# Kernel optimization log

Hardware: AMD Instinct MI355X
Metric: run time of the kernel (lower is better)

The kernel has to match this reference:

```python
import jax, jax.numpy as jnp
import numpy as np

SEQ, BATCH, IN, RES = 1024, 64, 512, 2048

def setup_inputs() -> dict:
    key = jax.random.key(0)
    k1, k2, k3, k4 = jax.random.split(key, 4)
    x = jax.random.normal(k1, (SEQ, BATCH, IN), dtype=jnp.float32)
    # ESN reservoir weights: untrained random matrices (spectral-radius style scaling)
    W_in = jax.random.normal(k2, (RES, IN), dtype=jnp.float32) * 0.1
    W_hh = jax.random.normal(k3, (RES, RES), dtype=jnp.float32) * (0.9 / jnp.sqrt(RES))
    b = jax.random.normal(k4, (RES,), dtype=jnp.float32) * 0.1
    return {"x": x, "W_in": W_in, "W_hh": W_hh, "b": b}

def reference(x, W_in, W_hh, b):
    # ESNBase.forward -> _forward_type_2 with num_layers=1, unidirectional.
    # h_t = tanh(x_t @ W_in^T + h_{t-1} @ W_hh^T + b)
    batch = x.shape[1]
    h0 = jnp.zeros((batch, W_hh.shape[0]), dtype=x.dtype)
    # Precompute input projection for all steps (parallel GEMM), scan the recurrence.
    xin = jnp.einsum('sbi,ri->sbr', x, W_in) + b  # (seq, batch, res)
    def step(h, u):
        h_new = jnp.tanh(u + h @ W_hh.T)
        return h_new, h_new
    h_n, states = jax.lax.scan(step, h0, xin)
    # output: (seq, batch, num_directions*hidden); h_n: (num_layers*num_directions, batch, hidden)
    return states, h_n[None, :, :]
```

## Files before the change

### kernel.cpp

```cpp
#include <hip/hip_runtime.h>
#include <hip/hip_bf16.h>


#define SEQ  1024
#define NB   64
#define INF  512
#define RES  2048
#define RING 16

typedef float    f32x4 __attribute__((ext_vector_type(4)));
typedef _Float16 f16x8 __attribute__((ext_vector_type(8)));

__device__ __forceinline__ float fast_tanh(float x) {
  const float e = __expf(2.0f * x);
  return 1.0f - 2.0f * __builtin_amdgcn_rcpf(1.0f + e);
}

__global__ __launch_bounds__(256) void xin_gemm(
    const float* __restrict__ X, const float* __restrict__ Win,
    const float* __restrict__ bias, float* __restrict__ U)
{
  __shared__ _Float16 lA[2][128][40];
  __shared__ _Float16 lB[2][128][40];

  const int tid  = threadIdx.x;
  const int lane = tid & 63;
  const int wv   = tid >> 6;
  const int wr   = wv >> 1;
  const int wc   = wv & 1;
  const int m0   = (blockIdx.x >> 4) * 128;
  const int n0   = (blockIdx.x & 15) * 128;

  const int srow = tid >> 1;
  const int sk   = (tid & 1) * 16;

  const int fr = lane & 15;
  const int fk = (lane >> 4) * 8;

  f32x4 acc[4][4] = {};
  float ra[16], rb[16];

  const float* xa_base = X   + (size_t)(m0 + srow) * INF + sk;
  const float* xb_base = Win + (size_t)(n0 + srow) * INF + sk;

#define LOADK(kt) do {                                                     \
    const float* pa = xa_base + (kt) * 32;                                 \
    const float* pb = xb_base + (kt) * 32;                                 \
    *(f32x4*)&ra[0]  = *(const f32x4*)(pa + 0);                            \
    *(f32x4*)&ra[4]  = *(const f32x4*)(pa + 4);                            \
    *(f32x4*)&ra[8]  = *(const f32x4*)(pa + 8);                            \
    *(f32x4*)&ra[12] = *(const f32x4*)(pa + 12);                           \
    *(f32x4*)&rb[0]  = *(const f32x4*)(pb + 0);                            \
    *(f32x4*)&rb[4]  = *(const f32x4*)(pb + 4);                            \
    *(f32x4*)&rb[8]  = *(const f32x4*)(pb + 8);                            \
    *(f32x4*)&rb[12] = *(const f32x4*)(pb + 12);                           \
  } while (0)

#define STOREK(buf) do {                                                   \
    f16x8 h0, h1;                                                          \
    _Pragma("unroll") for (int j = 0; j < 8; ++j) h0[j] = (_Float16)ra[j]; \
    _Pragma("unroll") for (int j = 0; j < 8; ++j) h1[j] = (_Float16)ra[8+j];\
    *(f16x8*)&lA[buf][srow][sk]     = h0;                                  \
    *(f16x8*)&lA[buf][srow][sk + 8] = h1;                                  \
    _Pragma("unroll") for (int j = 0; j < 8; ++j) h0[j] = (_Float16)rb[j]; \
    _Pragma("unroll") for (int j = 0; j < 8; ++j) h1[j] = (_Float16)rb[8+j];\
    *(f16x8*)&lB[buf][srow][sk]     = h0;                                  \
    *(f16x8*)&lB[buf][srow][sk + 8] = h1;                                  \
  } while (0)

#define COMPUTE(buf) do {                                                  \
    f16x8 af[4], bf[4];                                                    \
    _Pragma("unroll") for (int mt = 0; mt < 4; ++mt)                       \
      af[mt] = *(const f16x8*)&lA[buf][wr*64 + mt*16 + fr][fk];            \
    _Pragma("unroll") for (int nt = 0; nt < 4; ++nt)                       \
      bf[nt] = *(const f16x8*)&lB[buf][wc*64 + nt*16 + fr][fk];            \
    _Pragma("unroll") for (int mt = 0; mt < 4; ++mt)                       \
      _Pragma("unroll") for (int nt = 0; nt < 4; ++nt)                     \
        acc[mt][nt] = __builtin_amdgcn_mfma_f32_16x16x32_f16(              \
            af[mt], bf[nt], acc[mt][nt], 0, 0, 0);                         \
  } while (0)

  LOADK(0);
  STOREK(0);
  __syncthreads();

#pragma unroll 1
  for (int kt = 0; kt < 16; ++kt) {
    const int buf = kt & 1;
    if (kt < 15) LOADK(kt + 1);
    COMPUTE(buf);
    if (kt < 15) STOREK(buf ^ 1);
    __syncthreads();
  }

#pragma unroll
  for (int mt = 0; mt < 4; ++mt) {
    const int row = m0 + wr*64 + mt*16 + (lane >> 4) * 4;
#pragma unroll
    for (int nt = 0; nt < 4; ++nt) {
      const int col = n0 + wc*64 + nt*16 + fr;
      const float bv = bias[col];
#pragma unroll
      for (int i = 0; i < 4; ++i)
        U[(size_t)(row + i) * RES + col] = acc[mt][nt][i] + bv;
    }
  }
#undef LOADK
#undef STOREK
#undef COMPUTE
}

__global__ __launch_bounds__(512, 1) void esn_recur(
    const float* __restrict__ Whh, float* __restrict__ states,
    float* __restrict__ hn, _Float16* __restrict__ ring,
    unsigned* __restrict__ flags)
{
  __shared__ f32x4 red0[8][64];
  __shared__ f32x4 red1[8][64];

  const int tid  = threadIdx.x;
  const int lane = tid & 63;
  const int wv   = tid >> 6;
  const int q    = wv;

  const int bid = blockIdx.x;
  const int xg  = bid & 7;
  const int bg  = xg >> 1;
  const int cg  = ((xg & 1) << 5) | (bid >> 3);
  const int b0  = bg * 16;
  const int c0  = cg * 32;

  const int fr = lane & 15;
  const int fk = (lane >> 4) * 8;

  f16x8 wf[2][8];
#pragma unroll
  for (int ct = 0; ct < 2; ++ct) {
#pragma unroll
    for (int ks = 0; ks < 8; ++ks) {
      const float* wsrc = Whh + (size_t)(c0 + ct*16 + fr) * RES
                        + q*256 + ks*32 + fk;
      const f32x4 w0 = *(const f32x4*)(wsrc);
      const f32x4 w1 = *(const f32x4*)(wsrc + 4);
      f16x8 f;
#pragma unroll
      for (int j = 0; j < 4; ++j) { f[j] = (_Float16)w0[j]; f[4+j] = (_Float16)w1[j]; }
      wf[ct][ks] = f;
    }
  }

  unsigned* const fb = flags + bg * (128 * 32);

  for (int s = 0; s < SEQ; ++s) {
    f32x4 a0 = {0.f, 0.f, 0.f, 0.f}, a1 = {0.f, 0.f, 0.f, 0.f};

    float u[4];
    if (wv < 2) {
      const float* up = states + (size_t)s * NB * RES;
      const int col = c0 + wv * 16 + fr;
#pragma unroll
      for (int i = 0; i < 4; ++i)
        u[i] = up[(size_t)(b0 + (lane >> 4) * 4 + i) * RES + col];
    }

    if (s > 0) {
      const _Float16* hp = ring + (size_t)((s - 1) & (RING - 1)) * NB * RES
                         + (size_t)(b0 + fr) * RES + q * 256 + fk;
      f16x8 hv[8];
      for (;;) {
#pragma unroll
        for (int ks = 0; ks < 8; ++ks) {
          union { unsigned long long w[2]; f16x8 v; } au;
          au.w[0] = __hip_atomic_load((const unsigned long long*)(hp + ks*32),
                                      __ATOMIC_RELAXED, __HIP_MEMORY_SCOPE_AGENT);
          au.w[1] = __hip_atomic_load((const unsigned long long*)(hp + ks*32 + 4),
                                      __ATOMIC_RELAXED, __HIP_MEMORY_SCOPE_AGENT);
          hv[ks] = au.v;
        }
        f16x8 t0 = hv[0] + hv[1], t1 = hv[2] + hv[3];
        f16x8 t2 = hv[4] + hv[5], t3 = hv[6] + hv[7];
        f16x8 ss = (t0 + t1) + (t2 + t3);
        union { f16x8 v; unsigned w[4]; } su; su.v = ss;
        unsigned bad = 0;
#pragma unroll
        for (int j = 0; j < 4; ++j) {
          bad |= ((su.w[j] & 0x7C00u) == 0x7C00u);
          bad |= (((su.w[j] >> 16) & 0x7C00u) == 0x7C00u);
        }
        if (!__any(bad)) break;
      }
#pragma unroll
      for (int ks = 0; ks < 8; ++ks) {
        a0 = __builtin_amdgcn_mfma_f32_16x16x32_f16(hv[ks], wf[0][ks], a0, 0, 0, 0);
        a1 = __builtin_amdgcn_mfma_f32_16x16x32_f16(hv[ks], wf[1][ks], a1, 0, 0, 0);
      }
    }

    red0[q][lane] = a0;
    red1[q][lane] = a1;
    __syncthreads();

    const bool barrier_step = ((s & 7) == 7) && (s != SEQ - 1);

    if (wv < 2) {
      const f32x4 (* __restrict__ rp)[64] = wv ? red1 : red0;
      f32x4 acc = rp[0][lane];
#pragma unroll
      for (int j = 1; j < 8; ++j) acc += rp[j][lane];

      float* up = states + (size_t)s * NB * RES;
      unsigned short* hc16 = (unsigned short*)(ring
                           + (size_t)(s & (RING - 1)) * NB * RES);
      const int col = c0 + wv * 16 + fr;
#pragma unroll
      for (int i = 0; i < 4; ++i) {
        const int b = b0 + (lane >> 4) * 4 + i;
        const size_t off = (size_t)b * RES + col;
        const float v = fast_tanh(u[i] + acc[i]);
        up[off] = v;
        const _Float16 vh = (_Float16)v;
        __hip_atomic_store(&hc16[off], __builtin_bit_cast(unsigned short, vh),
                           __ATOMIC_RELAXED, __HIP_MEMORY_SCOPE_AGENT);
        if (s == SEQ - 1) hn[off] = v;
      }
      asm volatile("s_waitcnt vmcnt(0)" ::: "memory");

      if (barrier_step) {
#pragma unroll
        for (int d = 1; d <= 8; ++d) {
          unsigned short* pz = (unsigned short*)(ring
                             + (size_t)((s + d) & (RING - 1)) * NB * RES);
#pragma unroll
          for (int i = 0; i < 4; ++i) {
            const size_t off = (size_t)(b0 + (lane >> 4) * 4 + i) * RES + col;
            __hip_atomic_store(&pz[off], (unsigned short)0x7F7Fu,
                               __ATOMIC_RELAXED, __HIP_MEMORY_SCOPE_AGENT);
          }
        }
        asm volatile("s_waitcnt vmcnt(0)" ::: "memory");
        if (lane == 0)
          __hip_atomic_store(fb + (wv * 64 + cg) * 32, (unsigned)((s >> 3) + 1),
                             __ATOMIC_RELAXED, __HIP_MEMORY_SCOPE_AGENT);
      }
    } else if (wv == 2 && barrier_step) {
      const unsigned tgt = (unsigned)((s >> 3) + 1);
      for (;;) {
        const unsigned va = __hip_atomic_load(fb + lane * 32,
                              __ATOMIC_RELAXED, __HIP_MEMORY_SCOPE_AGENT);
        const unsigned vb = __hip_atomic_load(fb + (64 + lane) * 32,
                              __ATOMIC_RELAXED, __HIP_MEMORY_SCOPE_AGENT);
        if (__all((va >= tgt) & (vb >= tgt))) break;
      }
    }
    __syncthreads();
  }
}

extern "C" void kernel_launch(void* const* d_in, const int* in_sizes, int n_in,
                              void* d_out, int out_size, void* d_ws, size_t ws_size,
                              hipStream_t stream) {
  const float* x    = (const float*)d_in[0];
  const float* W_in = (const float*)d_in[1];
  const float* W_hh = (const float*)d_in[2];
  const float* bias = (const float*)d_in[3];

  float* states = (float*)d_out;
  float* hn     = states + (size_t)SEQ * NB * RES;

  _Float16* ring  = (_Float16*)d_ws;
  unsigned* flags = (unsigned*)((char*)d_ws
                  + (size_t)RING * NB * RES * sizeof(_Float16));

  hipMemsetAsync(ring, 0x7F, (size_t)RING * NB * RES * sizeof(_Float16), stream);
  hipMemsetAsync(flags, 0, (size_t)4 * 128 * 32 * sizeof(unsigned), stream);

  xin_gemm<<<dim3(512 * 16), dim3(256), 0, stream>>>(x, W_in, bias, states);
  esn_recur<<<dim3(256), dim3(512), 0, stream>>>(W_hh, states, hn, ring, flags);
}
```

Baseline: 6.679 ms.

## Replace flag barriers with ring-slot poisoning and LDS-staged hidden state

Reworks the persistent recurrence kernel's partition. Each block now owns 8 batch rows and 64 columns. Waves cooperatively load the previous hidden state into LDS and then feed MFMA from LDS, split into four K-quarters with a cross-wave reduction. The periodic global flag barrier is removed. Instead, spare waves re-poison the ring slot four steps ahead every step, and the ring shrinks to 8 slots. This cuts global polling and the 8-step group sync, but it relies on the 4-step lead being enough to avoid races. It also wastes half the MFMA rows, since only 8 of the 16 rows are valid.

```diff
diff --git a/kernel.cpp b/kernel.cpp
--- a/kernel.cpp
+++ b/kernel.cpp
@@ -6,7 +6,7 @@
 #define NB   64
 #define INF  512
 #define RES  2048
-#define RING 16
+#define RING 8
 
 typedef float    f32x4 __attribute__((ext_vector_type(4)));
 typedef _Float16 f16x8 __attribute__((ext_vector_type(8)));
@@ -110,76 +110,70 @@
 #undef COMPUTE
 }
 
-__global__ __launch_bounds__(512, 1) void esn_recur(
+__global__ __launch_bounds__(512, 2) void esn_recur(
     const float* __restrict__ Whh, float* __restrict__ states,
-    float* __restrict__ hn, _Float16* __restrict__ ring,
-    unsigned* __restrict__ flags)
+    float* __restrict__ hn, _Float16* __restrict__ ring)
 {
-  __shared__ f32x4 red0[8][64];
-  __shared__ f32x4 red1[8][64];
+  __shared__ _Float16 hl[8 * 2056];
+  __shared__ f32x4    red[2][3][2][2][64];
 
   const int tid  = threadIdx.x;
   const int lane = tid & 63;
   const int wv   = tid >> 6;
-  const int q    = wv;
+  const int kQ   = wv >> 1;
+  const int ctH  = wv & 1;
 
   const int bid = blockIdx.x;
-  const int xg  = bid & 7;
-  const int bg  = xg >> 1;
-  const int cg  = ((xg & 1) << 5) | (bid >> 3);
-  const int b0  = bg * 16;
-  const int c0  = cg * 32;
+  const int g   = bid & 7;
+  const int b0  = g * 8;
+  const int c0  = (bid >> 3) * 64;
 
   const int fr = lane & 15;
   const int fk = (lane >> 4) * 8;
 
-  f16x8 wf[2][8];
-#pragma unroll
-  for (int ct = 0; ct < 2; ++ct) {
-#pragma unroll
-    for (int ks = 0; ks < 8; ++ks) {
-      const float* wsrc = Whh + (size_t)(c0 + ct*16 + fr) * RES
-                        + q*256 + ks*32 + fk;
-      const f32x4 w0 = *(const f32x4*)(wsrc);
-      const f32x4 w1 = *(const f32x4*)(wsrc + 4);
+  f16x8 wf[2][16];
+#pragma unroll 1
+  for (int ct2 = 0; ct2 < 2; ++ct2)
+#pragma unroll
+    for (int ks = 0; ks < 16; ++ks) {
+      const float* src = Whh + (size_t)(c0 + (ctH*2 + ct2)*16 + fr) * RES
+                       + kQ*512 + ks*32 + fk;
+      const f32x4 w0 = *(const f32x4*)src;
+      const f32x4 w1 = *(const f32x4*)(src + 4);
       f16x8 f;
 #pragma unroll
       for (int j = 0; j < 4; ++j) { f[j] = (_Float16)w0[j]; f[4+j] = (_Float16)w1[j]; }
-      wf[ct][ks] = f;
-    }
-  }
-
-  unsigned* const fb = flags + bg * (128 * 32);
+      wf[ct2][ks] = f;
+    }
+
+  const bool epi = (kQ == 0) && ((lane >> 4) < 2);
 
   for (int s = 0; s < SEQ; ++s) {
-    f32x4 a0 = {0.f, 0.f, 0.f, 0.f}, a1 = {0.f, 0.f, 0.f, 0.f};
-
-    float u[4];
-    if (wv < 2) {
+    float u[2][4];
+    if (epi) {
       const float* up = states + (size_t)s * NB * RES;
-      const int col = c0 + wv * 16 + fr;
-#pragma unroll
-      for (int i = 0; i < 4; ++i)
-        u[i] = up[(size_t)(b0 + (lane >> 4) * 4 + i) * RES + col];
-    }
-
+#pragma unroll
+      for (int ct2 = 0; ct2 < 2; ++ct2) {
+        const int col = c0 + (ctH*2 + ct2)*16 + fr;
+#pragma unroll
+        for (int i = 0; i < 4; ++i)
+          u[ct2][i] = up[(size_t)(b0 + (lane >> 4)*4 + i) * RES + col];
+      }
+    }
+
+    unsigned long long d[8];
     if (s > 0) {
-      const _Float16* hp = ring + (size_t)((s - 1) & (RING - 1)) * NB * RES
-                         + (size_t)(b0 + fr) * RES + q * 256 + fk;
-      f16x8 hv[8];
+      const _Float16* hp = ring + (size_t)((s - 1) & (RING - 1)) * (NB * RES)
+                         + (size_t)(b0 + wv) * RES + lane * 32;
       for (;;) {
 #pragma unroll
-        for (int ks = 0; ks < 8; ++ks) {
-          union { unsigned long long w[2]; f16x8 v; } au;
-          au.w[0] = __hip_atomic_load((const unsigned long long*)(hp + ks*32),
-                                      __ATOMIC_RELAXED, __HIP_MEMORY_SCOPE_AGENT);
-          au.w[1] = __hip_atomic_load((const unsigned long long*)(hp + ks*32 + 4),
-                                      __ATOMIC_RELAXED, __HIP_MEMORY_SCOPE_AGENT);
-          hv[ks] = au.v;
-        }
-        f16x8 t0 = hv[0] + hv[1], t1 = hv[2] + hv[3];
-        f16x8 t2 = hv[4] + hv[5], t3 = hv[6] + hv[7];
-        f16x8 ss = (t0 + t1) + (t2 + t3);
+        for (int k = 0; k < 8; ++k)
+          d[k] = __hip_atomic_load((const unsigned long long*)hp + k,
+                                   __ATOMIC_RELAXED, __HIP_MEMORY_SCOPE_AGENT);
+        union { unsigned long long q[2]; f16x8 v; } p0, p1, p2, p3;
+        p0.q[0]=d[0]; p0.q[1]=d[1]; p1.q[0]=d[2]; p1.q[1]=d[3];
+        p2.q[0]=d[4]; p2.q[1]=d[5]; p3.q[0]=d[6]; p3.q[1]=d[7];
+        const f16x8 ss = (p0.v + p1.v) + (p2.v + p3.v);
         union { f16x8 v; unsigned w[4]; } su; su.v = ss;
         unsigned bad = 0;
 #pragma unroll
@@ -189,70 +183,71 @@
         }
         if (!__any(bad)) break;
       }
-#pragma unroll
-      for (int ks = 0; ks < 8; ++ks) {
-        a0 = __builtin_amdgcn_mfma_f32_16x16x32_f16(hv[ks], wf[0][ks], a0, 0, 0, 0);
-        a1 = __builtin_amdgcn_mfma_f32_16x16x32_f16(hv[ks], wf[1][ks], a1, 0, 0, 0);
-      }
-    }
-
-    red0[q][lane] = a0;
-    red1[q][lane] = a1;
+      _Float16* dst = hl + wv * 2056 + lane * 32;
+#pragma unroll
+      for (int k = 0; k < 4; ++k) {
+        union { unsigned long long q[2]; f16x8 v; } p;
+        p.q[0] = d[2*k]; p.q[1] = d[2*k + 1];
+        *(f16x8*)(dst + k * 8) = p.v;
+      }
+    }
     __syncthreads();
 
-    const bool barrier_step = ((s & 7) == 7) && (s != SEQ - 1);
-
-    if (wv < 2) {
-      const f32x4 (* __restrict__ rp)[64] = wv ? red1 : red0;
-      f32x4 acc = rp[0][lane];
-#pragma unroll
-      for (int j = 1; j < 8; ++j) acc += rp[j][lane];
-
-      float* up = states + (size_t)s * NB * RES;
-      unsigned short* hc16 = (unsigned short*)(ring
-                           + (size_t)(s & (RING - 1)) * NB * RES);
-      const int col = c0 + wv * 16 + fr;
-#pragma unroll
-      for (int i = 0; i < 4; ++i) {
-        const int b = b0 + (lane >> 4) * 4 + i;
-        const size_t off = (size_t)b * RES + col;
-        const float v = fast_tanh(u[i] + acc[i]);
-        up[off] = v;
-        const _Float16 vh = (_Float16)v;
-        __hip_atomic_store(&hc16[off], __builtin_bit_cast(unsigned short, vh),
-                           __ATOMIC_RELAXED, __HIP_MEMORY_SCOPE_AGENT);
-        if (s == SEQ - 1) hn[off] = v;
-      }
-      asm volatile("s_waitcnt vmcnt(0)" ::: "memory");
-
-      if (barrier_step) {
-#pragma unroll
-        for (int d = 1; d <= 8; ++d) {
-          unsigned short* pz = (unsigned short*)(ring
-                             + (size_t)((s + d) & (RING - 1)) * NB * RES);
+    f32x4 acc0 = {0.f, 0.f, 0.f, 0.f}, acc1 = {0.f, 0.f, 0.f, 0.f};
+    if (s > 0) {
+      const int  arow = lane & 15;
+      const bool av   = arow < 8;
+      const _Float16* ab = hl + arow * 2056 + kQ * 512 + fk;
+#pragma unroll
+      for (int ks = 0; ks < 16; ++ks) {
+        f16x8 a = {};
+        if (av) a = *(const f16x8*)(ab + ks * 32);
+        acc0 = __builtin_amdgcn_mfma_f32_16x16x32_f16(a, wf[0][ks], acc0, 0, 0, 0);
+        acc1 = __builtin_amdgcn_mfma_f32_16x16x32_f16(a, wf[1][ks], acc1, 0, 0, 0);
+      }
+    }
+
+    if (kQ > 0) {
+      red[s & 1][kQ - 1][ctH][0][lane] = acc0;
+      red[s & 1][kQ - 1][ctH][1][lane] = acc1;
+    }
+    __syncthreads();
+
+    if (kQ == 0) {
+#pragma unroll
+      for (int j = 0; j < 3; ++j) {
+        acc0 += red[s & 1][j][ctH][0][lane];
+        acc1 += red[s & 1][j][ctH][1][lane];
+      }
+      if (epi) {
+        float* up = states + (size_t)s * NB * RES;
+        unsigned short* hc = (unsigned short*)(ring
+                           + (size_t)(s & (RING - 1)) * (NB * RES));
+#pragma unroll
+        for (int ct2 = 0; ct2 < 2; ++ct2) {
+          const int col = c0 + (ctH*2 + ct2)*16 + fr;
+          const f32x4 a = ct2 ? acc1 : acc0;
 #pragma unroll
           for (int i = 0; i < 4; ++i) {
-            const size_t off = (size_t)(b0 + (lane >> 4) * 4 + i) * RES + col;
-            __hip_atomic_store(&pz[off], (unsigned short)0x7F7Fu,
+            const int r = (lane >> 4) * 4 + i;
+            const size_t off = (size_t)(b0 + r) * RES + col;
+            const float v = fast_tanh(u[ct2][i] + a[i]);
+            up[off] = v;
+            const _Float16 vh = (_Float16)v;
+            __hip_atomic_store(hc + off, __builtin_bit_cast(unsigned short, vh),
                                __ATOMIC_RELAXED, __HIP_MEMORY_SCOPE_AGENT);
+            if (s == SEQ - 1) hn[off] = v;
           }
         }
-        asm volatile("s_waitcnt vmcnt(0)" ::: "memory");
-        if (lane == 0)
-          __hip_atomic_store(fb + (wv * 64 + cg) * 32, (unsigned)((s >> 3) + 1),
-                             __ATOMIC_RELAXED, __HIP_MEMORY_SCOPE_AGENT);
-      }
-    } else if (wv == 2 && barrier_step) {
-      const unsigned tgt = (unsigned)((s >> 3) + 1);
-      for (;;) {
-        const unsigned va = __hip_atomic_load(fb + lane * 32,
-                              __ATOMIC_RELAXED, __HIP_MEMORY_SCOPE_AGENT);
-        const unsigned vb = __hip_atomic_load(fb + (64 + lane) * 32,
-                              __ATOMIC_RELAXED, __HIP_MEMORY_SCOPE_AGENT);
-        if (__all((va >= tgt) & (vb >= tgt))) break;
-      }
-    }
-    __syncthreads();
+      }
+    } else if (kQ >= 2) {
+      const int j   = wv - 4;
+      const int row = 2*j + (lane >> 5);
+      unsigned* pz = (unsigned*)(ring + (size_t)((s + 4) & (RING - 1)) * (NB * RES)
+                   + (size_t)(b0 + row) * RES + c0);
+      __hip_atomic_store(pz + (lane & 31), 0x7F7F7F7Fu,
+                         __ATOMIC_RELAXED, __HIP_MEMORY_SCOPE_AGENT);
+    }
   }
 }
 
@@ -267,13 +262,10 @@
   float* states = (float*)d_out;
   float* hn     = states + (size_t)SEQ * NB * RES;
 
-  _Float16* ring  = (_Float16*)d_ws;
-  unsigned* flags = (unsigned*)((char*)d_ws
-                  + (size_t)RING * NB * RES * sizeof(_Float16));
+  _Float16* ring = (_Float16*)d_ws;
 
   hipMemsetAsync(ring, 0x7F, (size_t)RING * NB * RES * sizeof(_Float16), stream);
-  hipMemsetAsync(flags, 0, (size_t)4 * 128 * 32 * sizeof(unsigned), stream);
 
   xin_gemm<<<dim3(512 * 16), dim3(256), 0, stream>>>(x, W_in, bias, states);
-  esn_recur<<<dim3(256), dim3(512), 0, stream>>>(W_hh, states, hn, ring, flags);
-}
+  esn_recur<<<dim3(256), dim3(512), 0, stream>>>(W_hh, states, hn, ring);
+}
```

Measured after the change: 26.26 ms. 293% more time.
